# Optimization experiments

Hardware: AMD Instinct MI355X
Metric: run time of the kernel (lower is better)

Reference implementation:

```python
import jax, jax.numpy as jnp
import numpy as np

N_NODES = 50000
N_EDGES = 640000
NODE_DIM = 16
HIDDEN = 128
LATENT = 64
MAX_NODES = 100
NUM_GRAPHS = 256


def _xavier(key, fan_in, fan_out):
    bound = np.sqrt(6.0 / (fan_in + fan_out)).astype(np.float32)
    return jax.random.uniform(key, (fan_in, fan_out), jnp.float32, -bound, bound)


def setup_inputs() -> dict:
    key = jax.random.key(0)
    ks = jax.random.split(key, 16)
    inp = {
        "x": jax.random.normal(ks[0], (N_NODES, NODE_DIM), jnp.float32),
        "edge_index": jax.random.randint(ks[1], (2, N_EDGES), 0, N_NODES, jnp.int64),
        "batch": jnp.sort(jax.random.randint(ks[2], (N_NODES,), 0, NUM_GRAPHS, jnp.int64)),
        "eps": jax.random.normal(ks[3], (NUM_GRAPHS, LATENT), jnp.float32),
        # conv1 MLP
        "w1a": _xavier(ks[4], NODE_DIM, HIDDEN), "b1a": jnp.zeros((HIDDEN,), jnp.float32),
        "w1b": _xavier(ks[5], HIDDEN, HIDDEN), "b1b": jnp.zeros((HIDDEN,), jnp.float32),
        # conv2 MLP
        "w2a": _xavier(ks[6], HIDDEN, HIDDEN), "b2a": jnp.zeros((HIDDEN,), jnp.float32),
        "w2b": _xavier(ks[7], HIDDEN, HIDDEN), "b2b": jnp.zeros((HIDDEN,), jnp.float32),
        # heads
        "wmu": _xavier(ks[8], HIDDEN, LATENT), "bmu": jnp.zeros((LATENT,), jnp.float32),
        "wlv": _xavier(ks[9], HIDDEN, LATENT), "blv": jnp.zeros((LATENT,), jnp.float32),
        # decoder
        "wd1": _xavier(ks[10], LATENT, HIDDEN), "bd1": jnp.zeros((HIDDEN,), jnp.float32),
        "wd2": _xavier(ks[11], HIDDEN, HIDDEN), "bd2": jnp.zeros((HIDDEN,), jnp.float32),
        "wn": _xavier(ks[12], HIDDEN, MAX_NODES * NODE_DIM), "bn": jnp.zeros((MAX_NODES * NODE_DIM,), jnp.float32),
        "we": _xavier(ks[13], HIDDEN, MAX_NODES * MAX_NODES), "be": jnp.zeros((MAX_NODES * MAX_NODES,), jnp.float32),
    }
    return inp


def _gin(x, src, dst, wa, ba, wb, bb):
    # GIN with eps=0: MLP(x + sum_{j->i} x_j)
    agg = jax.ops.segment_sum(x[src], dst, num_segments=N_NODES) + x
    h = jax.nn.relu(agg @ wa + ba)
    return h @ wb + bb


def reference(x, edge_index, batch, eps,
              w1a, b1a, w1b, b1b, w2a, b2a, w2b, b2b,
              wmu, bmu, wlv, blv, wd1, bd1, wd2, bd2, wn, bn, we, be):
    src, dst = edge_index[0], edge_index[1]
    # encode
    h = jax.nn.relu(_gin(x, src, dst, w1a, b1a, w1b, b1b))
    h = jax.nn.relu(_gin(h, src, dst, w2a, b2a, w2b, b2b))
    summed = jax.ops.segment_sum(h, batch, num_segments=NUM_GRAPHS)
    counts = jax.ops.segment_sum(jnp.ones((N_NODES,), h.dtype), batch, num_segments=NUM_GRAPHS)
    pooled = summed / jnp.maximum(counts, 1.0)[:, None]
    mu = pooled @ wmu + bmu
    logvar = jnp.clip(pooled @ wlv + blv, -5.0, 5.0)
    # reparameterize
    z = mu + eps * jnp.exp(0.5 * logvar)
    # decode
    hd = jax.nn.relu(z @ wd1 + bd1) @ wd2 + bd2
    node_features = jax.nn.softmax((hd @ wn + bn).reshape(NUM_GRAPHS, MAX_NODES, NODE_DIM), axis=-1)
    adj = (hd @ we + be).reshape(NUM_GRAPHS, MAX_NODES, MAX_NODES)
    adj = (adj + jnp.swapaxes(adj, -1, -2)) * 0.5
    eye = jnp.eye(MAX_NODES, dtype=bool)
    adj = jnp.where(eye[None], -10.0, adj)
    adj = jnp.clip(adj, -10.0, 10.0)
    return adj, node_features, mu, logvar
```

## Files before the change

### kernel.cpp

```cpp
#include <hip/hip_runtime.h>
#include <hip/hip_bf16.h>

#define N_NODES   50000
#define N_EDGES   640000
#define NODE_DIM  16
#define HIDDEN    128
#define LATENT    64
#define MAX_NODES 100
#define NUM_GRAPHS 256

typedef unsigned short ushort_t;
typedef unsigned int   uint_t;
typedef short  short8 __attribute__((ext_vector_type(8)));
typedef float  f32x4  __attribute__((ext_vector_type(4)));

__device__ __forceinline__ float bf2f(ushort_t u) {
    return __uint_as_float(((uint_t)u) << 16);
}
__device__ __forceinline__ ushort_t f2bf(float f) {
    const uint_t u = __float_as_uint(f);
    return (ushort_t)((u + 0x7fffu + ((u >> 16) & 1u)) >> 16);
}

__device__ __forceinline__ void mfma_acc(f32x4& acc, short8 a, short8 b) {
    asm volatile("v_mfma_f32_16x16x32_bf16 %0, %1, %2, %0"
                 : "+v"(acc) : "v"(a), "v"(b));
}
__device__ __forceinline__ void mfma_hazard_wait() {
    asm volatile("s_nop 7\n\ts_nop 7");
}

__global__ void degree_kernel(const int* __restrict__ dst, int* __restrict__ deg) {
    const int i0 = (blockIdx.x * blockDim.x + threadIdx.x) * 4;
    if (i0 + 4 <= N_EDGES) {
        const int4 d = *(const int4*)&dst[i0];
        atomicAdd(&deg[d.x], 1);
        atomicAdd(&deg[d.y], 1);
        atomicAdd(&deg[d.z], 1);
        atomicAdd(&deg[d.w], 1);
    }
}

__global__ void blockscan_kernel(const int* __restrict__ deg,
                                 int* __restrict__ row_start,
                                 int* __restrict__ blocksum) {
    __shared__ int s_wave[16];
    const int tid  = threadIdx.x;
    const int lane = tid & 63;
    const int wid  = tid >> 6;
    const int idx  = blockIdx.x * 1024 + tid;

    const int v = (idx < N_NODES) ? deg[idx] : 0;
    int x = v;
    #pragma unroll
    for (int o = 1; o < 64; o <<= 1) {
        const int y = __shfl_up(x, o);
        if (lane >= o) x += y;
    }
    if (lane == 63) s_wave[wid] = x;
    __syncthreads();
    if (tid == 0) {
        int run = 0;
        #pragma unroll
        for (int w = 0; w < 16; ++w) { const int t = s_wave[w]; s_wave[w] = run; run += t; }
        blocksum[blockIdx.x] = run;
    }
    __syncthreads();
    if (idx < N_NODES) row_start[idx] = s_wave[wid] + x - v;
}

__global__ void scan_fixup_kernel(int* __restrict__ row_start,
                                  int* __restrict__ cursor,
                                  const int* __restrict__ blocksum) {
    __shared__ int s_off;
    const int bid = blockIdx.x;
    const int tid = threadIdx.x;
    if (tid < 64) {
        int v = (tid < bid) ? blocksum[tid] : 0;
        #pragma unroll
        for (int o = 32; o > 0; o >>= 1) v += __shfl_down(v, o);
        if (tid == 0) s_off = v;
    }
    __syncthreads();
    const int idx = bid * 1024 + tid;
    if (idx < N_NODES) {
        const int r = row_start[idx] + s_off;
        row_start[idx] = r;
        cursor[idx] = r;
    }
    if (bid == 0 && tid == 0) row_start[N_NODES] = N_EDGES;
}

__global__ void csr_fill_kernel(const int* __restrict__ src,
                                const int* __restrict__ dst,
                                int* __restrict__ cursor,
                                int* __restrict__ nbr) {
    const int i0 = (blockIdx.x * blockDim.x + threadIdx.x) * 4;
    if (i0 + 4 <= N_EDGES) {
        const int4 d = *(const int4*)&dst[i0];
        const int4 s = *(const int4*)&src[i0];
        const int p0 = atomicAdd(&cursor[d.x], 1);
        const int p1 = atomicAdd(&cursor[d.y], 1);
        const int p2 = atomicAdd(&cursor[d.z], 1);
        const int p3 = atomicAdd(&cursor[d.w], 1);
        nbr[p0] = s.x; nbr[p1] = s.y; nbr[p2] = s.z; nbr[p3] = s.w;
    }
}

__global__ void pack_w3_kernel(const float* __restrict__ wA, ushort_t* __restrict__ oA,
                               const float* __restrict__ wB, ushort_t* __restrict__ oB,
                               const float* __restrict__ wC, ushort_t* __restrict__ oC) {
    const int gid = blockIdx.x * blockDim.x + threadIdx.x;
    const int sel = gid >> 14;
    const int idx = gid & 16383;
    const float* w = (sel == 0) ? wA : (sel == 1) ? wB : wC;
    ushort_t* out  = (sel == 0) ? oA : (sel == 1) ? oB : oC;
    const int j    = idx & 7;
    const int lane = (idx >> 3) & 63;
    const int kb   = (idx >> 9) & 3;
    const int nt   = idx >> 11;
    const int k = kb * 32 + ((lane >> 4) << 3) + j;
    const int n = (nt << 4) + (lane & 15);
    out[idx] = f2bf(w[k * HIDDEN + n]);
}

__global__ void gin1_fused_kernel(const float* __restrict__ in,
                                  const int* __restrict__ row_start,
                                  const int* __restrict__ nbr,
                                  const float* __restrict__ wa, const float* __restrict__ ba,
                                  const ushort_t* __restrict__ wpkb, const float* __restrict__ bb,
                                  ushort_t* __restrict__ out) {
    __shared__ float s_in[16][NODE_DIM + 1];
    __shared__ __align__(16) ushort_t s_mid[16][HIDDEN + 8];
    const int tid = threadIdx.x;
    const int n0  = blockIdx.x * 16;

    {
        const int grp = tid >> 4;
        const int k   = tid & 15;
        #pragma unroll
        for (int half = 0; half < 2; ++half) {
            const int i = grp + half * 8;
            const int n = n0 + i;
            const int beg = row_start[n], end = row_start[n + 1];
            float a0 = in[(long)n * NODE_DIM + k], a1 = 0.f, a2 = 0.f, a3 = 0.f;
            int p = beg;
            for (; p + 4 <= end; p += 4) {
                const int e0 = nbr[p], e1 = nbr[p + 1], e2 = nbr[p + 2], e3 = nbr[p + 3];
                a0 += in[(long)e0 * NODE_DIM + k];
                a1 += in[(long)e1 * NODE_DIM + k];
                a2 += in[(long)e2 * NODE_DIM + k];
                a3 += in[(long)e3 * NODE_DIM + k];
            }
            for (; p < end; ++p) a0 += in[(long)nbr[p] * NODE_DIM + k];
            s_in[i][k] = (a0 + a1) + (a2 + a3);
        }
    }
    __syncthreads();

    {
        const int dq = tid & 31;  const int d0 = dq * 4;
        const int iq = tid >> 5;  const int i0 = iq * 4;
        float acc[4][4];
        const float4 bv = *(const float4*)&ba[d0];
        #pragma unroll
        for (int j = 0; j < 4; ++j) {
            acc[j][0] = bv.x; acc[j][1] = bv.y; acc[j][2] = bv.z; acc[j][3] = bv.w;
        }
        for (int k = 0; k < NODE_DIM; ++k) {
            const float4 w = *(const float4*)&wa[k * HIDDEN + d0];
            #pragma unroll
            for (int j = 0; j < 4; ++j) {
                const float a = s_in[i0 + j][k];
                acc[j][0] += a * w.x; acc[j][1] += a * w.y;
                acc[j][2] += a * w.z; acc[j][3] += a * w.w;
            }
        }
        #pragma unroll
        for (int j = 0; j < 4; ++j) {
            ushort4 v;
            v.x = f2bf(fmaxf(acc[j][0], 0.f)); v.y = f2bf(fmaxf(acc[j][1], 0.f));
            v.z = f2bf(fmaxf(acc[j][2], 0.f)); v.w = f2bf(fmaxf(acc[j][3], 0.f));
            *(ushort4*)&s_mid[i0 + j][d0] = v;
        }
    }
    __syncthreads();

    {
        const int lane = tid & 63;
        const int wv   = tid >> 6;
        short8 afr[4];
        #pragma unroll
        for (int kb = 0; kb < 4; ++kb)
            afr[kb] = *(const short8*)&s_mid[lane & 15][kb * 32 + ((lane >> 4) << 3)];
        const int col = lane & 15;
        const int r0  = (lane >> 4) << 2;
        #pragma unroll
        for (int t = 0; t < 4; ++t) {
            const int nt = wv * 4 + t;
            short8 bfr[4];
            #pragma unroll
            for (int kb = 0; kb < 4; ++kb)
                bfr[kb] = *(const short8*)&wpkb[(((nt << 2) | kb) << 9) + (lane << 3)];
            f32x4 acc = {0.f, 0.f, 0.f, 0.f};
            #pragma unroll
            for (int kb = 0; kb < 4; ++kb) mfma_acc(acc, afr[kb], bfr[kb]);
            mfma_hazard_wait();
            const float bias = bb[nt * 16 + col];
            #pragma unroll
            for (int r = 0; r < 4; ++r)
                out[(long)(n0 + r0 + r) * HIDDEN + nt * 16 + col] =
                    f2bf(fmaxf(acc[r] + bias, 0.f));
        }
    }
}

__global__ void gin2_fused_kernel(const ushort_t* __restrict__ in,
                                  const int* __restrict__ row_start,
                                  const int* __restrict__ nbr,
                                  const ushort_t* __restrict__ wpka, const float* __restrict__ ba,
                                  const ushort_t* __restrict__ wpkb, const float* __restrict__ bb,
                                  float* __restrict__ out) {
    __shared__ __align__(16) ushort_t s_in[16][HIDDEN + 8];
    __shared__ __align__(16) ushort_t s_mid[16][HIDDEN + 8];
    const int tid  = threadIdx.x;
    const int lane = tid & 63;
    const int wv   = tid >> 6;
    const int n0   = blockIdx.x * 16;

    {
        const int d2 = lane * 2;
        #pragma unroll
        for (int t = 0; t < 8; ++t) {
            const int i = wv * 8 + t;
            const int n = n0 + i;
            const int beg = row_start[n], end = row_start[n + 1];
            const uint_t sv = *(const uint_t*)&in[(long)n * HIDDEN + d2];
            float ax[8], ay[8];
            ax[0] = bf2f(sv & 0xffffu); ay[0] = bf2f(sv >> 16);
            #pragma unroll
            for (int q = 1; q < 8; ++q) { ax[q] = 0.f; ay[q] = 0.f; }
            int p = beg;
            for (; p + 8 <= end; p += 8) {
                uint_t v[8];
                #pragma unroll
                for (int q = 0; q < 8; ++q)
                    v[q] = *(const uint_t*)&in[(long)nbr[p + q] * HIDDEN + d2];
                #pragma unroll
                for (int q = 0; q < 8; ++q) {
                    ax[q] += bf2f(v[q] & 0xffffu); ay[q] += bf2f(v[q] >> 16);
                }
            }
            for (; p + 2 <= end; p += 2) {
                const uint_t v0 = *(const uint_t*)&in[(long)nbr[p]     * HIDDEN + d2];
                const uint_t v1 = *(const uint_t*)&in[(long)nbr[p + 1] * HIDDEN + d2];
                ax[0] += bf2f(v0 & 0xffffu); ay[0] += bf2f(v0 >> 16);
                ax[1] += bf2f(v1 & 0xffffu); ay[1] += bf2f(v1 >> 16);
            }
            if (p < end) {
                const uint_t v0 = *(const uint_t*)&in[(long)nbr[p] * HIDDEN + d2];
                ax[0] += bf2f(v0 & 0xffffu); ay[0] += bf2f(v0 >> 16);
            }
            const float rx = ((ax[0] + ax[1]) + (ax[2] + ax[3])) + ((ax[4] + ax[5]) + (ax[6] + ax[7]));
            const float ry = ((ay[0] + ay[1]) + (ay[2] + ay[3])) + ((ay[4] + ay[5]) + (ay[6] + ay[7]));
            const uint_t packed = (uint_t)f2bf(rx) | ((uint_t)f2bf(ry) << 16);
            *(uint_t*)&s_in[i][d2] = packed;
        }
    }
    __syncthreads();

    const int col = lane & 15;
    const int r0  = (lane >> 4) << 2;

    {
        short8 afr[4];
        #pragma unroll
        for (int kb = 0; kb < 4; ++kb)
            afr[kb] = *(const short8*)&s_in[lane & 15][kb * 32 + ((lane >> 4) << 3)];
        #pragma unroll
        for (int t = 0; t < 4; ++t) {
            const int nt = wv * 4 + t;
            short8 bfr[4];
            #pragma unroll
            for (int kb = 0; kb < 4; ++kb)
                bfr[kb] = *(const short8*)&wpka[(((nt << 2) | kb) << 9) + (lane << 3)];
            f32x4 acc = {0.f, 0.f, 0.f, 0.f};
            #pragma unroll
            for (int kb = 0; kb < 4; ++kb) mfma_acc(acc, afr[kb], bfr[kb]);
            mfma_hazard_wait();
            const float bias = ba[nt * 16 + col];
            #pragma unroll
            for (int r = 0; r < 4; ++r)
                s_mid[r0 + r][nt * 16 + col] = f2bf(fmaxf(acc[r] + bias, 0.f));
        }
    }
    __syncthreads();

    {
        short8 afr[4];
        #pragma unroll
        for (int kb = 0; kb < 4; ++kb)
            afr[kb] = *(const short8*)&s_mid[lane & 15][kb * 32 + ((lane >> 4) << 3)];
        #pragma unroll
        for (int t = 0; t < 4; ++t) {
            const int nt = wv * 4 + t;
            short8 bfr[4];
            #pragma unroll
            for (int kb = 0; kb < 4; ++kb)
                bfr[kb] = *(const short8*)&wpkb[(((nt << 2) | kb) << 9) + (lane << 3)];
            f32x4 acc = {0.f, 0.f, 0.f, 0.f};
            #pragma unroll
            for (int kb = 0; kb < 4; ++kb) mfma_acc(acc, afr[kb], bfr[kb]);
            mfma_hazard_wait();
            const float bias = bb[nt * 16 + col];
            #pragma unroll
            for (int r = 0; r < 4; ++r)
                out[(long)(n0 + r0 + r) * HIDDEN + nt * 16 + col] =
                    fmaxf(acc[r] + bias, 0.f);
        }
    }
}

__global__ void pool_kernel(const float* __restrict__ h,
                            const int* __restrict__ batch,
                            float* __restrict__ summed,
                            float* __restrict__ counts) {
    const int NPB = 32;
    const int n0 = blockIdx.x * NPB;
    if (n0 >= N_NODES) return;
    const int nend = min(n0 + NPB, N_NODES);
    const int d = threadIdx.x;

    int cur = batch[n0];
    float acc = 0.f;
    int cnt = 0;
    for (int n = n0; n < nend; ++n) {
        const int g = batch[n];
        if (g != cur) {
            atomicAdd(&summed[cur * HIDDEN + d], acc);
            if (d == 0) atomicAdd(&counts[cur], (float)cnt);
            acc = 0.f; cnt = 0; cur = g;
        }
        acc += h[(long)n * HIDDEN + d];
        ++cnt;
    }
    atomicAdd(&summed[cur * HIDDEN + d], acc);
    if (d == 0) atomicAdd(&counts[cur], (float)cnt);
}

__global__ void head_kernel(const float* __restrict__ summed,
                            const float* __restrict__ counts,
                            const float* __restrict__ eps,
                            const float* __restrict__ wmu, const float* __restrict__ bmu,
                            const float* __restrict__ wlv, const float* __restrict__ blv,
                            const float* __restrict__ wd1, const float* __restrict__ bd1,
                            const float* __restrict__ wd2, const float* __restrict__ bd2,
                            float* __restrict__ out_mu, float* __restrict__ out_lv,
                            float* __restrict__ hd) {
    const int g = blockIdx.x;
    const int d = threadIdx.x;
    __shared__ float s_pool[HIDDEN];
    __shared__ float s_z[LATENT];
    __shared__ float s_h1[HIDDEN];

    const float cnt = fmaxf(counts[g], 1.f);
    s_pool[d] = summed[g * HIDDEN + d] / cnt;
    __syncthreads();

    if (d < LATENT) {
        float m = bmu[d], lv = blv[d];
        for (int k = 0; k < HIDDEN; ++k) {
            const float p = s_pool[k];
            m  += p * wmu[k * LATENT + d];
            lv += p * wlv[k * LATENT + d];
        }
        lv = fminf(fmaxf(lv, -5.f), 5.f);
        out_mu[g * LATENT + d] = m;
        out_lv[g * LATENT + d] = lv;
        s_z[d] = m + eps[g * LATENT + d] * expf(0.5f * lv);
    }
    __syncthreads();
    {
        float a = bd1[d];
        for (int k = 0; k < LATENT; ++k) a += s_z[k] * wd1[k * HIDDEN + d];
        s_h1[d] = fmaxf(a, 0.f);
    }
    __syncthreads();
    {
        float a = bd2[d];
        for (int k = 0; k < HIDDEN; ++k) a += s_h1[k] * wd2[k * HIDDEN + d];
        hd[g * HIDDEN + d] = a;
    }
}

#define GB2 16
#define ADJ_BLOCKS 40
__global__ void decoder_gemm2_kernel(const float* __restrict__ hd,
                                     const float* __restrict__ we, const float* __restrict__ be,
                                     float* __restrict__ raw_adj,
                                     const float* __restrict__ wn, const float* __restrict__ bn,
                                     float* __restrict__ raw_nf) {
    const int g0 = blockIdx.y * GB2;
    const bool is_adj = (blockIdx.x < ADJ_BLOCKS);
    const float* W    = is_adj ? we : wn;
    const float* bias = is_adj ? be : bn;
    float* raw        = is_adj ? raw_adj : raw_nf;
    const int N       = is_adj ? (MAX_NODES * MAX_NODES) : (MAX_NODES * NODE_DIM);
    const int bx      = is_adj ? blockIdx.x : blockIdx.x - ADJ_BLOCKS;
    const int cg = threadIdx.x & 63;
    const int gg = threadIdx.x >> 6;
    const int o0 = bx * 256 + cg * 4;

    __shared__ float s_hd[GB2][HIDDEN];
    for (int idx = threadIdx.x; idx < GB2 * HIDDEN; idx += 256) {
        s_hd[idx >> 7][idx & 127] = hd[(long)(g0 + (idx >> 7)) * HIDDEN + (idx & 127)];
    }
    __syncthreads();
    if (o0 >= N) return;

    float4 acc[4];
    const float4 bv = *(const float4*)&bias[o0];
    #pragma unroll
    for (int j = 0; j < 4; ++j) acc[j] = bv;

    for (int k0 = 0; k0 < HIDDEN; k0 += 8) {
        float4 w[8];
        #pragma unroll
        for (int u = 0; u < 8; ++u)
            w[u] = *(const float4*)&W[(long)(k0 + u) * N + o0];
        #pragma unroll
        for (int u = 0; u < 8; ++u) {
            #pragma unroll
            for (int j = 0; j < 4; ++j) {
                const float a = s_hd[gg * 4 + j][k0 + u];
                acc[j].x += a * w[u].x; acc[j].y += a * w[u].y;
                acc[j].z += a * w[u].z; acc[j].w += a * w[u].w;
            }
        }
    }
    #pragma unroll
    for (int j = 0; j < 4; ++j)
        *(float4*)&raw[(long)(g0 + gg * 4 + j) * N + o0] = acc[j];
}

__global__ void epilogue_kernel(const float* __restrict__ raw_adj,
                                float* __restrict__ out_adj,
                                const float* __restrict__ raw_nf,
                                float* __restrict__ out_nf) {
    const int tid = threadIdx.x;
    if (blockIdx.x < NUM_GRAPHS) {
        const int g = blockIdx.x;
        __shared__ float s_a[MAX_NODES * MAX_NODES];
        const float* r = raw_adj + (long)g * MAX_NODES * MAX_NODES;
        for (int o = tid; o < MAX_NODES * MAX_NODES; o += blockDim.x) s_a[o] = r[o];
        __syncthreads();
        float* w = out_adj + (long)g * MAX_NODES * MAX_NODES;
        for (int o = tid; o < MAX_NODES * MAX_NODES; o += blockDim.x) {
            const int i = o / MAX_NODES;
            const int j = o - i * MAX_NODES;
            float v;
            if (i == j) v = -10.f;
            else        v = fminf(fmaxf(0.5f * (s_a[o] + s_a[j * MAX_NODES + i]), -10.f), 10.f);
            w[o] = v;
        }
    } else {
        const int idx = (blockIdx.x - NUM_GRAPHS) * blockDim.x + tid;
        if (idx >= NUM_GRAPHS * MAX_NODES) return;
        const float* r = raw_nf + (long)idx * NODE_DIM;
        float mx = -1e30f;
        #pragma unroll
        for (int d = 0; d < NODE_DIM; ++d) mx = fmaxf(mx, r[d]);
        float e[NODE_DIM];
        float s = 0.f;
        #pragma unroll
        for (int d = 0; d < NODE_DIM; ++d) { e[d] = expf(r[d] - mx); s += e[d]; }
        const float inv = 1.f / s;
        float* w = out_nf + (long)idx * NODE_DIM;
        #pragma unroll
        for (int d = 0; d < NODE_DIM; ++d) w[d] = e[d] * inv;
    }
}

extern "C" void kernel_launch(void* const* d_in, const int* in_sizes, int n_in,
                              void* d_out, int out_size, void* d_ws, size_t ws_size,
                              hipStream_t stream) {
    const float* x    = (const float*)d_in[0];
    const int*   edge = (const int*)d_in[1];
    const int*   src  = edge;
    const int*   dst  = edge + N_EDGES;
    const int*   batch = (const int*)d_in[2];
    const float* eps  = (const float*)d_in[3];
    const float* w1a = (const float*)d_in[4],  *b1a = (const float*)d_in[5];
    const float* w1b = (const float*)d_in[6],  *b1b = (const float*)d_in[7];
    const float* w2a = (const float*)d_in[8],  *b2a = (const float*)d_in[9];
    const float* w2b = (const float*)d_in[10], *b2b = (const float*)d_in[11];
    const float* wmu = (const float*)d_in[12], *bmu = (const float*)d_in[13];
    const float* wlv = (const float*)d_in[14], *blv = (const float*)d_in[15];
    const float* wd1 = (const float*)d_in[16], *bd1 = (const float*)d_in[17];
    const float* wd2 = (const float*)d_in[18], *bd2 = (const float*)d_in[19];
    const float* wn  = (const float*)d_in[20], *bn  = (const float*)d_in[21];
    const float* we  = (const float*)d_in[22], *be  = (const float*)d_in[23];

    float* out = (float*)d_out;
    float* out_adj = out;
    float* out_nf  = out + (long)NUM_GRAPHS * MAX_NODES * MAX_NODES;
    float* out_mu  = out_nf + (long)NUM_GRAPHS * MAX_NODES * NODE_DIM;
    float* out_lv  = out_mu + NUM_GRAPHS * LATENT;

    float* ws = (float*)d_ws;
    ushort_t* h1 = (ushort_t*)ws;
    float* h2     = ws + 3200000;
    float* summed = h2 + (long)N_NODES * HIDDEN;
    float* counts = summed + NUM_GRAPHS * HIDDEN;
    float* hd     = counts + NUM_GRAPHS;
    int*   deg       = (int*)(hd + NUM_GRAPHS * HIDDEN);
    int*   row_start = deg + N_NODES;
    int*   cursor    = row_start + N_NODES + 1;
    int*   nbr       = cursor + N_NODES;
    int*   blocksum  = nbr + N_EDGES;
    ushort_t* wpk1b = (ushort_t*)(((uintptr_t)(blocksum + 64) + 15) & ~(uintptr_t)15);
    ushort_t* wpk2a = wpk1b + HIDDEN * HIDDEN;
    ushort_t* wpk2b = wpk2a + HIDDEN * HIDDEN;
    float* raw_adj = (float*)h1;
    float* raw_nf  = (float*)h1 + (long)NUM_GRAPHS * MAX_NODES * MAX_NODES;

    hipMemsetAsync(deg, 0, sizeof(int) * N_NODES, stream);
    degree_kernel<<<N_EDGES / 4 / 256, 256, 0, stream>>>(dst, deg);
    blockscan_kernel<<<(N_NODES + 1023) / 1024, 1024, 0, stream>>>(deg, row_start, blocksum);
    scan_fixup_kernel<<<(N_NODES + 1023) / 1024, 1024, 0, stream>>>(row_start, cursor, blocksum);
    csr_fill_kernel<<<N_EDGES / 4 / 256, 256, 0, stream>>>(src, dst, cursor, nbr);
    pack_w3_kernel<<<192, 256, 0, stream>>>(w1b, wpk1b, w2a, wpk2a, w2b, wpk2b);

    gin1_fused_kernel<<<N_NODES / 16, 128, 0, stream>>>(x, row_start, nbr,
                                                        w1a, b1a, wpk1b, b1b, h1);
    gin2_fused_kernel<<<N_NODES / 16, 128, 0, stream>>>(h1, row_start, nbr,
                                                        wpk2a, b2a, wpk2b, b2b, h2);

    hipMemsetAsync(summed, 0, sizeof(float) * (NUM_GRAPHS * HIDDEN + NUM_GRAPHS), stream);
    pool_kernel<<<(N_NODES + 31) / 32, 128, 0, stream>>>(h2, batch, summed, counts);

    head_kernel<<<NUM_GRAPHS, 128, 0, stream>>>(summed, counts, eps,
                                                wmu, bmu, wlv, blv,
                                                wd1, bd1, wd2, bd2,
                                                out_mu, out_lv, hd);

    {
        dim3 grid(ADJ_BLOCKS + 7, NUM_GRAPHS / GB2);
        decoder_gemm2_kernel<<<grid, 256, 0, stream>>>(hd, we, be, raw_adj,
                                                       wn, bn, raw_nf);
    }

    epilogue_kernel<<<NUM_GRAPHS + 50, 512, 0, stream>>>(raw_adj, out_adj,
                                                         raw_nf, out_nf);
}
```

Measured before the change: 196.7 us.

## Fuse mean-pool segment sum into GIN2 epilogue and drop h2 buffer

New measurement: 205.0 us. 1.04x slower.

```diff
diff --git a/kernel.cpp b/kernel.cpp
--- a/kernel.cpp
+++ b/kernel.cpp
@@ -71,7 +71,8 @@
 
 __global__ void scan_fixup_kernel(int* __restrict__ row_start,
                                   int* __restrict__ cursor,
-                                  const int* __restrict__ blocksum) {
+                                  const int* __restrict__ blocksum,
+                                  float* __restrict__ summed) {
     __shared__ int s_off;
     const int bid = blockIdx.x;
     const int tid = threadIdx.x;
@@ -88,6 +89,7 @@
         row_start[idx] = r;
         cursor[idx] = r;
     }
+    if (idx < NUM_GRAPHS * HIDDEN) summed[idx] = 0.f;
     if (bid == 0 && tid == 0) row_start[N_NODES] = N_EDGES;
 }
 
@@ -218,15 +220,20 @@
 __global__ void gin2_fused_kernel(const ushort_t* __restrict__ in,
                                   const int* __restrict__ row_start,
                                   const int* __restrict__ nbr,
+                                  const int* __restrict__ batch,
                                   const ushort_t* __restrict__ wpka, const float* __restrict__ ba,
                                   const ushort_t* __restrict__ wpkb, const float* __restrict__ bb,
-                                  float* __restrict__ out) {
+                                  float* __restrict__ summed) {
     __shared__ __align__(16) ushort_t s_in[16][HIDDEN + 8];
     __shared__ __align__(16) ushort_t s_mid[16][HIDDEN + 8];
+    __shared__ float s_h2[16][HIDDEN + 1];
+    __shared__ int s_b[16];
     const int tid  = threadIdx.x;
     const int lane = tid & 63;
     const int wv   = tid >> 6;
     const int n0   = blockIdx.x * 16;
+
+    if (tid < 16) s_b[tid] = batch[n0 + tid];
 
     {
         const int d2 = lane * 2;
@@ -315,41 +322,30 @@
             const float bias = bb[nt * 16 + col];
             #pragma unroll
             for (int r = 0; r < 4; ++r)
-                out[(long)(n0 + r0 + r) * HIDDEN + nt * 16 + col] =
-                    fmaxf(acc[r] + bias, 0.f);
-        }
-    }
-}
-
-__global__ void pool_kernel(const float* __restrict__ h,
+                s_h2[r0 + r][nt * 16 + col] = fmaxf(acc[r] + bias, 0.f);
+        }
+    }
+    __syncthreads();
+
+    {
+        const int d = tid & 127;
+        int cur = s_b[0];
+        float acc = 0.f;
+        #pragma unroll
+        for (int i = 0; i < 16; ++i) {
+            const int g = s_b[i];
+            if (g != cur) {
+                atomicAdd(&summed[cur * HIDDEN + d], acc);
+                acc = 0.f; cur = g;
+            }
+            acc += s_h2[i][d];
+        }
+        atomicAdd(&summed[cur * HIDDEN + d], acc);
+    }
+}
+
+__global__ void head_kernel(const float* __restrict__ summed,
                             const int* __restrict__ batch,
-                            float* __restrict__ summed,
-                            float* __restrict__ counts) {
-    const int NPB = 32;
-    const int n0 = blockIdx.x * NPB;
-    if (n0 >= N_NODES) return;
-    const int nend = min(n0 + NPB, N_NODES);
-    const int d = threadIdx.x;
-
-    int cur = batch[n0];
-    float acc = 0.f;
-    int cnt = 0;
-    for (int n = n0; n < nend; ++n) {
-        const int g = batch[n];
-        if (g != cur) {
-            atomicAdd(&summed[cur * HIDDEN + d], acc);
-            if (d == 0) atomicAdd(&counts[cur], (float)cnt);
-            acc = 0.f; cnt = 0; cur = g;
-        }
-        acc += h[(long)n * HIDDEN + d];
-        ++cnt;
-    }
-    atomicAdd(&summed[cur * HIDDEN + d], acc);
-    if (d == 0) atomicAdd(&counts[cur], (float)cnt);
-}
-
-__global__ void head_kernel(const float* __restrict__ summed,
-                            const float* __restrict__ counts,
                             const float* __restrict__ eps,
                             const float* __restrict__ wmu, const float* __restrict__ bmu,
                             const float* __restrict__ wlv, const float* __restrict__ blv,
@@ -362,9 +358,17 @@
     __shared__ float s_pool[HIDDEN];
     __shared__ float s_z[LATENT];
     __shared__ float s_h1[HIDDEN];
-
-    const float cnt = fmaxf(counts[g], 1.f);
-    s_pool[d] = summed[g * HIDDEN + d] / cnt;
+    __shared__ float s_cnt;
+
+    if (d == 0) {
+        int lo = 0, hi = N_NODES;
+        while (lo < hi) { const int m = (lo + hi) >> 1; if (batch[m] < g) lo = m + 1; else hi = m; }
+        int lo2 = lo, hi2 = N_NODES;
+        while (lo2 < hi2) { const int m = (lo2 + hi2) >> 1; if (batch[m] < g + 1) lo2 = m + 1; else hi2 = m; }
+        s_cnt = fmaxf((float)(lo2 - lo), 1.f);
+    }
+    __syncthreads();
+    s_pool[d] = summed[g * HIDDEN + d] / s_cnt;
     __syncthreads();
 
     if (d < LATENT) {
@@ -509,10 +513,8 @@
 
     float* ws = (float*)d_ws;
     ushort_t* h1 = (ushort_t*)ws;
-    float* h2     = ws + 3200000;
-    float* summed = h2 + (long)N_NODES * HIDDEN;
-    float* counts = summed + NUM_GRAPHS * HIDDEN;
-    float* hd     = counts + NUM_GRAPHS;
+    float* summed = ws + 3200000;
+    float* hd     = summed + NUM_GRAPHS * HIDDEN;
     int*   deg       = (int*)(hd + NUM_GRAPHS * HIDDEN);
     int*   row_start = deg + N_NODES;
     int*   cursor    = row_start + N_NODES + 1;
@@ -527,19 +529,17 @@
     hipMemsetAsync(deg, 0, sizeof(int) * N_NODES, stream);
     degree_kernel<<<N_EDGES / 4 / 256, 256, 0, stream>>>(dst, deg);
     blockscan_kernel<<<(N_NODES + 1023) / 1024, 1024, 0, stream>>>(deg, row_start, blocksum);
-    scan_fixup_kernel<<<(N_NODES + 1023) / 1024, 1024, 0, stream>>>(row_start, cursor, blocksum);
+    scan_fixup_kernel<<<(N_NODES + 1023) / 1024, 1024, 0, stream>>>(row_start, cursor,
+                                                                    blocksum, summed);
     csr_fill_kernel<<<N_EDGES / 4 / 256, 256, 0, stream>>>(src, dst, cursor, nbr);
     pack_w3_kernel<<<192, 256, 0, stream>>>(w1b, wpk1b, w2a, wpk2a, w2b, wpk2b);
 
     gin1_fused_kernel<<<N_NODES / 16, 128, 0, stream>>>(x, row_start, nbr,
                                                         w1a, b1a, wpk1b, b1b, h1);
-    gin2_fused_kernel<<<N_NODES / 16, 128, 0, stream>>>(h1, row_start, nbr,
-                                                        wpk2a, b2a, wpk2b, b2b, h2);
-
-    hipMemsetAsync(summed, 0, sizeof(float) * (NUM_GRAPHS * HIDDEN + NUM_GRAPHS), stream);
-    pool_kernel<<<(N_NODES + 31) / 32, 128, 0, stream>>>(h2, batch, summed, counts);
-
-    head_kernel<<<NUM_GRAPHS, 128, 0, stream>>>(summed, counts, eps,
+    gin2_fused_kernel<<<N_NODES / 16, 128, 0, stream>>>(h1, row_start, nbr, batch,
+                                                        wpk2a, b2a, wpk2b, b2b, summed);
+
+    head_kernel<<<NUM_GRAPHS, 128, 0, stream>>>(summed, batch, eps,
                                                 wmu, bmu, wlv, blv,
                                                 wd1, bd1, wd2, bd2,
                                                 out_mu, out_lv, hd);
```
